# Optimization experiments

Hardware: AMD Instinct MI355X
Metric: run time of the kernel (lower is better)

The kernel has to match this reference:

```python
import jax, jax.numpy as jnp
import numpy as np

N_NODES = 100000
N_EDGES = 1600000
IN_FEATS = 128
N_HIDDEN = 128
N_CLASSES = 47


def setup_inputs() -> dict:
    key = jax.random.key(0)
    ks = jax.random.split(key, 9)
    x = jax.random.normal(ks[0], (N_NODES, IN_FEATS), dtype=jnp.float32)
    src = jax.random.randint(ks[1], (N_EDGES,), 0, N_NODES, dtype=jnp.int32)
    dst = jax.random.randint(ks[2], (N_EDGES,), 0, N_NODES, dtype=jnp.int32)
    s = 0.05
    return {
        "x": x, "src": src, "dst": dst,
        "Ws0": jax.random.normal(ks[3], (IN_FEATS, N_HIDDEN), jnp.float32) * s,
        "Wn0": jax.random.normal(ks[4], (IN_FEATS, N_HIDDEN), jnp.float32) * s,
        "b0": jnp.zeros((N_HIDDEN,), jnp.float32),
        "Ws1": jax.random.normal(ks[5], (N_HIDDEN, N_HIDDEN), jnp.float32) * s,
        "Wn1": jax.random.normal(ks[6], (N_HIDDEN, N_HIDDEN), jnp.float32) * s,
        "b1": jnp.zeros((N_HIDDEN,), jnp.float32),
        "Ws2": jax.random.normal(ks[7], (N_HIDDEN, N_CLASSES), jnp.float32) * s,
        "Wn2": jax.random.normal(ks[8], (N_HIDDEN, N_CLASSES), jnp.float32) * s,
        "b2": jnp.zeros((N_CLASSES,), jnp.float32),
    }


def _sage_layer(h, src, dst, inv_deg, Ws, Wn, b):
    # weighted (w=1) mean aggregation over in-neighbors: sum(h[src]) / in_degree
    msg = h[src]  # [E, d] irregular gather
    neigh = jax.ops.segment_sum(msg, dst, num_segments=N_NODES) * inv_deg[:, None]
    # DGL SAGEConv 'mean': fc_self(h_self) + fc_neigh(h_neigh), bias on self branch
    return h @ Ws + neigh @ Wn + b


def reference(x, src, dst, Ws0, Wn0, b0, Ws1, Wn1, b1, Ws2, Wn2, b2):
    deg = jax.ops.segment_sum(jnp.ones_like(dst, dtype=x.dtype), dst, num_segments=N_NODES)
    inv_deg = 1.0 / jnp.maximum(deg, 1.0)
    h = _sage_layer(x, src, dst, inv_deg, Ws0, Wn0, b0)
    h = jax.nn.relu(h)  # dropout is identity (eval / p=0)
    h = _sage_layer(h, src, dst, inv_deg, Ws1, Wn1, b1)
    h = jax.nn.relu(h)
    h = _sage_layer(h, src, dst, inv_deg, Ws2, Wn2, b2)
    return jax.nn.log_softmax(h, axis=-1)
```

## Files before the change

kernel.cpp:

```cpp
#include <hip/hip_runtime.h>
#include <hip/hip_bf16.h>

#define NN 100000
#define NE 1600000
#define F 128
#define NCLS 47

#define SCAN_B 98
#define NPB 256
#define BUCKETS 391
#define ABLK 512
#define ACHUNK (NE / ABLK)

typedef __attribute__((ext_vector_type(8))) short short8;
typedef __attribute__((ext_vector_type(8))) unsigned short u16x8;
typedef __attribute__((ext_vector_type(4))) float f32x4;

#define MFMA16(A, B, C) __builtin_amdgcn_mfma_f32_16x16x32_bf16(A, B, C, 0, 0, 0)

__device__ __forceinline__ unsigned short b16(float f) {
    unsigned int u = __builtin_bit_cast(unsigned int, f);
    unsigned int r = u + 0x7FFFu + ((u >> 16) & 1u);
    return (unsigned short)(r >> 16);
}
__device__ __forceinline__ float bflo(unsigned int u) { return __builtin_bit_cast(float, u << 16); }
__device__ __forceinline__ float bfhi(unsigned int u) { return __builtin_bit_cast(float, u & 0xFFFF0000u); }

__global__ void __launch_bounds__(256) k_bhist(const int* __restrict__ dst,
                                               int* __restrict__ bucket_cnt) {
    __shared__ int hist[BUCKETS];
    const int t = threadIdx.x;
    for (int i = t; i < BUCKETS; i += 256) hist[i] = 0;
    __syncthreads();
    const int e0 = blockIdx.x * ACHUNK;
    for (int i = t; i < ACHUNK; i += 256) atomicAdd(&hist[dst[e0 + i] >> 8], 1);
    __syncthreads();
    for (int i = t; i < BUCKETS; i += 256)
        if (hist[i]) atomicAdd(&bucket_cnt[i], hist[i]);
}

__global__ void k_bscan(const int* __restrict__ bucket_cnt, int* __restrict__ bucket_off,
                        int* __restrict__ cursor) {
    const int lane = threadIdx.x & 63;
    int run = 0;
#pragma unroll
    for (int c = 0; c < 7; c++) {
        int idx = c * 64 + lane;
        int v = (idx < BUCKETS) ? bucket_cnt[idx] : 0;
        int s = v;
#pragma unroll
        for (int off = 1; off < 64; off <<= 1) {
            int n = __shfl_up(s, off);
            if (lane >= off) s += n;
        }
        int excl = run + s - v;
        if (idx <= BUCKETS) {
            bucket_off[idx] = excl;
            cursor[idx] = excl;
        }
        run += __shfl(s, 63);
    }
}

__global__ void __launch_bounds__(256) k_bscatter(const int* __restrict__ src,
                                                  const int* __restrict__ dst,
                                                  int* __restrict__ cursor,
                                                  int2* __restrict__ ebuf) {
    __shared__ int hist[BUCKETS];
    __shared__ int base[BUCKETS];
    __shared__ int rank[BUCKETS];
    const int t = threadIdx.x;
    for (int i = t; i < BUCKETS; i += 256) {
        hist[i] = 0;
        rank[i] = 0;
    }
    __syncthreads();
    const int e0 = blockIdx.x * ACHUNK;
    for (int i = t; i < ACHUNK; i += 256) atomicAdd(&hist[dst[e0 + i] >> 8], 1);
    __syncthreads();
    for (int i = t; i < BUCKETS; i += 256) {
        int h = hist[i];
        base[i] = h ? atomicAdd(&cursor[i], h) : 0;
    }
    __syncthreads();
    for (int i = t; i < ACHUNK; i += 256) {
        int s = src[e0 + i];
        int d = dst[e0 + i];
        int b = d >> 8;
        int r = atomicAdd(&rank[b], 1);
        ebuf[base[b] + r] = make_int2(s, d);
    }
}

__global__ void __launch_bounds__(256) k_bdeg(const int2* __restrict__ ebuf,
                                              const int* __restrict__ bucket_off,
                                              int* __restrict__ deg) {
    __shared__ int cnt[NPB];
    const int t = threadIdx.x;
    cnt[t] = 0;
    __syncthreads();
    const int e0 = bucket_off[blockIdx.x], e1 = bucket_off[blockIdx.x + 1];
    for (int i = e0 + t; i < e1; i += 256) atomicAdd(&cnt[ebuf[i].y & 255], 1);
    __syncthreads();
    int node = (blockIdx.x << 8) + t;
    if (node < NN) deg[node] = cnt[t];
}

__global__ void __launch_bounds__(256) k_bfill(const int2* __restrict__ ebuf,
                                               const int* __restrict__ bucket_off,
                                               const int* __restrict__ row_off,
                                               int* __restrict__ col) {
    __shared__ int ro[NPB];
    __shared__ int cur[NPB];
    const int t = threadIdx.x;
    int node = (blockIdx.x << 8) + t;
    ro[t] = (node < NN) ? row_off[node] : 0;
    cur[t] = 0;
    __syncthreads();
    const int e0 = bucket_off[blockIdx.x], e1 = bucket_off[blockIdx.x + 1];
    for (int i = e0 + t; i < e1; i += 256) {
        int2 e = ebuf[i];
        int d = e.y & 255;
        int p = atomicAdd(&cur[d], 1);
        col[ro[d] + p] = e.x;
    }
}

__global__ void __launch_bounds__(256) k_part(const int* __restrict__ deg,
                                              int* __restrict__ partials) {
    __shared__ int ws[4];
    const int t = threadIdx.x, lane = t & 63, wid = t >> 6;
    int i0 = blockIdx.x * 1024 + t * 4;
    int s = 0;
    if (i0 + 3 < NN) {
        int4 v = *(const int4*)&deg[i0];
        s = v.x + v.y + v.z + v.w;
    } else {
#pragma unroll
        for (int j = 0; j < 4; j++) {
            int idx = i0 + j;
            if (idx < NN) s += deg[idx];
        }
    }
#pragma unroll
    for (int off = 1; off < 64; off <<= 1) s += __shfl_xor(s, off);
    if (lane == 0) ws[wid] = s;
    __syncthreads();
    if (t == 0) partials[blockIdx.x] = ws[0] + ws[1] + ws[2] + ws[3];
}

__global__ void k_scanpart(int* __restrict__ partials, int* __restrict__ row_off) {
    const int lane = threadIdx.x & 63;
    int v0 = (lane < SCAN_B) ? partials[lane] : 0;
    int i1 = lane + 64;
    int v1 = (i1 < SCAN_B) ? partials[i1] : 0;
    int s0 = v0;
#pragma unroll
    for (int off = 1; off < 64; off <<= 1) {
        int n = __shfl_up(s0, off);
        if (lane >= off) s0 += n;
    }
    int tot0 = __shfl(s0, 63);
    int s1 = v1;
#pragma unroll
    for (int off = 1; off < 64; off <<= 1) {
        int n = __shfl_up(s1, off);
        if (lane >= off) s1 += n;
    }
    if (lane < SCAN_B) partials[lane] = s0 - v0;
    if (i1 < SCAN_B) partials[i1] = tot0 + s1 - v1;
    if (lane == 0) row_off[NN] = NE;
}

__global__ void __launch_bounds__(256) k_offsets(const int* __restrict__ deg,
                                                 const int* __restrict__ partials,
                                                 int* __restrict__ row_off,
                                                 float* __restrict__ inv_deg) {
    __shared__ int wsum[4];
    const int t = threadIdx.x, lane = t & 63, wid = t >> 6;
    int i0 = blockIdx.x * 1024 + t * 4;
    int v[4];
    int loc = 0;
#pragma unroll
    for (int j = 0; j < 4; j++) {
        int idx = i0 + j;
        v[j] = (idx < NN) ? deg[idx] : 0;
        loc += v[j];
    }
    int run = loc;
#pragma unroll
    for (int off = 1; off < 64; off <<= 1) {
        int n = __shfl_up(run, off);
        if (lane >= off) run += n;
    }
    if (lane == 63) wsum[wid] = run;
    __syncthreads();
    int woff = partials[blockIdx.x];
#pragma unroll
    for (int wv = 0; wv < 4; wv++)
        if (wv < wid) woff += wsum[wv];
    int excl = woff + run - loc;
#pragma unroll
    for (int j = 0; j < 4; j++) {
        int idx = i0 + j;
        if (idx < NN) {
            row_off[idx] = excl;
            inv_deg[idx] = 1.0f / fmaxf((float)v[j], 1.0f);
            excl += v[j];
        }
    }
}

__global__ void k_cvt(const float* __restrict__ x, unsigned short* __restrict__ xb) {
    int t = blockIdx.x * blockDim.x + threadIdx.x;
    if (t >= NN * F / 8) return;
    const float4* x4 = (const float4*)x;
    float4 a = x4[t * 2], b = x4[t * 2 + 1];
    u16x8 o;
    o[0] = b16(a.x); o[1] = b16(a.y); o[2] = b16(a.z); o[3] = b16(a.w);
    o[4] = b16(b.x); o[5] = b16(b.y); o[6] = b16(b.z); o[7] = b16(b.w);
    ((u16x8*)xb)[t] = o;
}

__global__ void k_pack_all(const float* __restrict__ Ws0, const float* __restrict__ Wn0,
                           const float* __restrict__ Ws1, const float* __restrict__ Wn1,
                           const float* __restrict__ Ws2, const float* __restrict__ Wn2,
                           unsigned short* __restrict__ wp) {
    int idx = blockIdx.x * blockDim.x + threadIdx.x;
    if (idx >= 77824) return;
    const float* W;
    int base, ncols;
    if (idx < 65536) {
        int m = idx >> 14;
        W = (m == 0) ? Ws0 : (m == 1) ? Wn0 : (m == 2) ? Ws1 : Wn1;
        base = m << 14;
        ncols = 128;
    } else {
        int m = (idx - 65536) / 6144;
        W = m ? Wn2 : Ws2;
        base = 65536 + m * 6144;
        ncols = NCLS;
    }
    int li = idx - base;
    int nt = li >> 11;
    int r = li & 2047;
    int kk = r >> 9;
    int r2 = r & 511;
    int lane = r2 >> 3;
    int j = r2 & 7;
    int k = kk * 32 + ((lane >> 4) << 3) + j;
    int n = nt * 16 + (lane & 15);
    float v = (n < ncols) ? W[k * ncols + n] : 0.f;
    wp[idx] = b16(v);
}

__global__ void __launch_bounds__(256) k_aggb(const uint4* __restrict__ h4,
                                              const int* __restrict__ row_off,
                                              const int* __restrict__ col,
                                              const float* __restrict__ inv_deg,
                                              uint4* __restrict__ a4) {
    int node = (blockIdx.x * blockDim.x + threadIdx.x) >> 6;
    int lane = threadIdx.x & 63;
    if (node >= NN) return;
    int b = row_off[node], e = row_off[node + 1];
    int deg = e - b;
    const int g = lane >> 4, fl = lane & 15;
    float acc[8];
#pragma unroll
    for (int i = 0; i < 8; i++) acc[i] = 0.f;
    for (int base = 0; base < deg; base += 64) {
        int cnt = deg - base;
        if (cnt > 64) cnt = 64;
        int myc = col[b + base + (lane < cnt ? lane : 0)];
        for (int jj = 0; jj < cnt; jj += 16) {
            uint4 u[4];
#pragma unroll
            for (int k2 = 0; k2 < 4; k2++) {
                int r = jj + k2 * 4 + g;
                int c = __shfl(myc, r < cnt ? r : 0);
                u[k2] = h4[(size_t)(unsigned)c * 16u + fl];
            }
#pragma unroll
            for (int k2 = 0; k2 < 4; k2++) {
                int r = jj + k2 * 4 + g;
                unsigned m = (r < cnt) ? 0xFFFFFFFFu : 0u;
                uint4 v = u[k2];
                v.x &= m; v.y &= m; v.z &= m; v.w &= m;
                acc[0] += bflo(v.x); acc[1] += bfhi(v.x);
                acc[2] += bflo(v.y); acc[3] += bfhi(v.y);
                acc[4] += bflo(v.z); acc[5] += bfhi(v.z);
                acc[6] += bflo(v.w); acc[7] += bfhi(v.w);
            }
        }
    }
#pragma unroll
    for (int i = 0; i < 8; i++) {
        acc[i] += __shfl_xor(acc[i], 16);
        acc[i] += __shfl_xor(acc[i], 32);
    }
    if (g == 0) {
        float s = inv_deg[node];
        uint4 o;
        o.x = (unsigned)b16(acc[0] * s) | ((unsigned)b16(acc[1] * s) << 16);
        o.y = (unsigned)b16(acc[2] * s) | ((unsigned)b16(acc[3] * s) << 16);
        o.z = (unsigned)b16(acc[4] * s) | ((unsigned)b16(acc[5] * s) << 16);
        o.w = (unsigned)b16(acc[6] * s) | ((unsigned)b16(acc[7] * s) << 16);
        a4[(size_t)node * 16 + fl] = o;
    }
}

__global__ void __launch_bounds__(256) k_agg48(const uint4* __restrict__ hw4,
                                               const int* __restrict__ row_off,
                                               const int* __restrict__ col,
                                               const float* __restrict__ inv_deg,
                                               float4* __restrict__ aggf4) {
    int node = (blockIdx.x * blockDim.x + threadIdx.x) >> 6;
    int lane = threadIdx.x & 63;
    if (node >= NN) return;
    int b = row_off[node], e = row_off[node + 1];
    int deg = e - b;
    const int g = lane >> 3, fl = lane & 7;
    float acc[8];
#pragma unroll
    for (int i = 0; i < 8; i++) acc[i] = 0.f;
    for (int base = 0; base < deg; base += 64) {
        int cnt = deg - base;
        if (cnt > 64) cnt = 64;
        int myc = col[b + base + (lane < cnt ? lane : 0)];
        for (int jj = 0; jj < cnt; jj += 16) {
            uint4 u[2];
#pragma unroll
            for (int k2 = 0; k2 < 2; k2++) {
                int r = jj + k2 * 8 + g;
                int c = __shfl(myc, r < cnt ? r : 0);
                u[k2] = hw4[(size_t)(unsigned)c * 8u + fl];
            }
#pragma unroll
            for (int k2 = 0; k2 < 2; k2++) {
                int r = jj + k2 * 8 + g;
                unsigned m = (r < cnt) ? 0xFFFFFFFFu : 0u;
                uint4 v = u[k2];
                v.x &= m; v.y &= m; v.z &= m; v.w &= m;
                acc[0] += bflo(v.x); acc[1] += bfhi(v.x);
                acc[2] += bflo(v.y); acc[3] += bfhi(v.y);
                acc[4] += bflo(v.z); acc[5] += bfhi(v.z);
                acc[6] += bflo(v.w); acc[7] += bfhi(v.w);
            }
        }
    }
#pragma unroll
    for (int i = 0; i < 8; i++) {
        acc[i] += __shfl_xor(acc[i], 8);
        acc[i] += __shfl_xor(acc[i], 16);
        acc[i] += __shfl_xor(acc[i], 32);
    }
    if (lane < 8) {
        float s = inv_deg[node];
        float4 o0 = make_float4(acc[0] * s, acc[1] * s, acc[2] * s, acc[3] * s);
        float4 o1 = make_float4(acc[4] * s, acc[5] * s, acc[6] * s, acc[7] * s);
        aggf4[(size_t)node * 16 + fl * 2] = o0;
        aggf4[(size_t)node * 16 + fl * 2 + 1] = o1;
    }
}

template <bool RELU>
__global__ void __launch_bounds__(256) k_layer(const unsigned short* __restrict__ hb,
                                               const unsigned short* __restrict__ ab,
                                               const unsigned short* __restrict__ wps,
                                               const unsigned short* __restrict__ wpn,
                                               const float* __restrict__ bias,
                                               unsigned short* __restrict__ outb) {
    const int wid = threadIdx.x >> 6, lane = threadIdx.x & 63;
    const int tile0 = blockIdx.x * 64;
    const short8* ws8 = (const short8*)wps;
    const short8* wn8 = (const short8*)wpn;
    short8 wf[2][2][4];
#pragma unroll
    for (int t = 0; t < 2; t++) {
        int nt = 2 * wid + t;
#pragma unroll
        for (int kk = 0; kk < 4; kk++) {
            wf[0][t][kk] = ws8[(nt * 4 + kk) * 64 + lane];
            wf[1][t][kk] = wn8[(nt * 4 + kk) * 64 + lane];
        }
    }
    const int rb = lane & 15, kq = lane >> 4;
    float bv[2];
#pragma unroll
    for (int t = 0; t < 2; t++) bv[t] = bias[(2 * wid + t) * 16 + rb];
    const short8* h8 = (const short8*)hb;
    const short8* a8 = (const short8*)ab;
    f32x4 zero = {0.f, 0.f, 0.f, 0.f};
    f32x4 acc[4][2];
#pragma unroll
    for (int m = 0; m < 4; m++)
#pragma unroll
        for (int t = 0; t < 2; t++) acc[m][t] = zero;
#pragma unroll
    for (int kk = 0; kk < 4; kk++) {
#pragma unroll
        for (int m = 0; m < 4; m++) {
            int row = tile0 + m * 16 + rb;
            int rc = row < NN ? row : NN - 1;
            int idx = rc * 16 + kk * 4 + kq;
            short8 af = h8[idx];
            short8 gf = a8[idx];
            acc[m][0] = MFMA16(af, wf[0][0][kk], acc[m][0]);
            acc[m][1] = MFMA16(af, wf[0][1][kk], acc[m][1]);
            acc[m][0] = MFMA16(gf, wf[1][0][kk], acc[m][0]);
            acc[m][1] = MFMA16(gf, wf[1][1][kk], acc[m][1]);
        }
    }
#pragma unroll
    for (int m = 0; m < 4; m++) {
#pragma unroll
        for (int reg = 0; reg < 4; reg++) {
            int row = tile0 + m * 16 + kq * 4 + reg;
            if (row < NN) {
#pragma unroll
                for (int t = 0; t < 2; t++) {
                    float v = acc[m][t][reg] + bv[t];
                    if (RELU) v = fmaxf(v, 0.f);
                    outb[(size_t)row * F + (2 * wid + t) * 16 + rb] = b16(v);
                }
            }
        }
    }
}

__global__ void __launch_bounds__(512) k_nmul(const unsigned short* __restrict__ hb,
                                              const unsigned short* __restrict__ wpn,
                                              unsigned short* __restrict__ hw) {
    const int wid = threadIdx.x >> 6, lane = threadIdx.x & 63;
    const int R0 = blockIdx.x * 128 + wid * 16;
    const short8* wn8 = (const short8*)wpn;
    short8 wf[3][4];
#pragma unroll
    for (int nt = 0; nt < 3; nt++)
#pragma unroll
        for (int kk = 0; kk < 4; kk++) wf[nt][kk] = wn8[(nt * 4 + kk) * 64 + lane];
    const int rb = lane & 15, kq = lane >> 4;
    const short8* h8 = (const short8*)hb;
    f32x4 zero = {0.f, 0.f, 0.f, 0.f};
    f32x4 acc[3] = {zero, zero, zero};
    int rowr = R0 + rb;
    int rc = rowr < NN ? rowr : NN - 1;
#pragma unroll
    for (int kk = 0; kk < 4; kk++) {
        short8 af = h8[rc * 16 + kk * 4 + kq];
#pragma unroll
        for (int nt = 0; nt < 3; nt++) acc[nt] = MFMA16(af, wf[nt][kk], acc[nt]);
    }
#pragma unroll
    for (int reg = 0; reg < 4; reg++) {
        int row = R0 + kq * 4 + reg;
        if (row < NN) {
#pragma unroll
            for (int nt = 0; nt < 3; nt++)
                hw[(size_t)row * 64 + nt * 16 + rb] = b16(acc[nt][reg]);
        }
    }
}

__global__ void __launch_bounds__(512) k_out2(const unsigned short* __restrict__ hb,
                                              const float* __restrict__ aggf,
                                              const unsigned short* __restrict__ wps,
                                              const float* __restrict__ bias,
                                              float* __restrict__ out) {
    const int wid = threadIdx.x >> 6, lane = threadIdx.x & 63;
    const int R0 = blockIdx.x * 128 + wid * 16;
    const short8* ws8 = (const short8*)wps;
    short8 wf[3][4];
#pragma unroll
    for (int nt = 0; nt < 3; nt++)
#pragma unroll
        for (int kk = 0; kk < 4; kk++) wf[nt][kk] = ws8[(nt * 4 + kk) * 64 + lane];
    const int rb = lane & 15, kq = lane >> 4;
    float bv[3];
    bool valid[3];
#pragma unroll
    for (int nt = 0; nt < 3; nt++) {
        int c = nt * 16 + rb;
        valid[nt] = c < NCLS;
        bv[nt] = valid[nt] ? bias[c] : 0.f;
    }
    const short8* h8 = (const short8*)hb;
    f32x4 zero = {0.f, 0.f, 0.f, 0.f};
    f32x4 acc[3] = {zero, zero, zero};
    int rowr = R0 + rb;
    int rc = rowr < NN ? rowr : NN - 1;
#pragma unroll
    for (int kk = 0; kk < 4; kk++) {
        short8 af = h8[rc * 16 + kk * 4 + kq];
#pragma unroll
        for (int nt = 0; nt < 3; nt++) acc[nt] = MFMA16(af, wf[nt][kk], acc[nt]);
    }
#pragma unroll
    for (int reg = 0; reg < 4; reg++) {
        int row = R0 + kq * 4 + reg;
        int rc2 = row < NN ? row : NN - 1;
        float v[3];
        float mx = -1e30f;
#pragma unroll
        for (int nt = 0; nt < 3; nt++) {
            float av = aggf[(size_t)rc2 * 64 + nt * 16 + rb];
            v[nt] = acc[nt][reg] + av + bv[nt];
            if (valid[nt]) mx = fmaxf(mx, v[nt]);
        }
        for (int off = 1; off < 16; off <<= 1) mx = fmaxf(mx, __shfl_xor(mx, off));
        float s = 0.f;
#pragma unroll
        for (int nt = 0; nt < 3; nt++)
            if (valid[nt]) s += expf(v[nt] - mx);
        for (int off = 1; off < 16; off <<= 1) s += __shfl_xor(s, off);
        float L = mx + logf(s);
        if (row < NN) {
#pragma unroll
            for (int nt = 0; nt < 3; nt++)
                if (valid[nt]) out[(size_t)row * NCLS + nt * 16 + rb] = v[nt] - L;
        }
    }
}

extern "C" void kernel_launch(void* const* d_in, const int* in_sizes, int n_in,
                              void* d_out, int out_size, void* d_ws, size_t ws_size,
                              hipStream_t stream) {
    (void)in_sizes; (void)n_in; (void)out_size; (void)ws_size;
    const float* x = (const float*)d_in[0];
    const int* src = (const int*)d_in[1];
    const int* dst = (const int*)d_in[2];
    const float* Ws0 = (const float*)d_in[3];
    const float* Wn0 = (const float*)d_in[4];
    const float* b0 = (const float*)d_in[5];
    const float* Ws1 = (const float*)d_in[6];
    const float* Wn1 = (const float*)d_in[7];
    const float* b1 = (const float*)d_in[8];
    const float* Ws2 = (const float*)d_in[9];
    const float* Wn2 = (const float*)d_in[10];
    const float* b2 = (const float*)d_in[11];
    float* out = (float*)d_out;

    char* w = (char*)d_ws;
    size_t off = 0;
    auto alloc = [&](size_t bytes) -> char* {
        char* p = w + off;
        off = (off + bytes + 255) & ~(size_t)255;
        return p;
    };
    int* deg = (int*)alloc((size_t)NN * 4);
    int* row_off = (int*)alloc((size_t)(NN + 1) * 4);
    int* col = (int*)alloc((size_t)NE * 4);
    float* inv_deg = (float*)alloc((size_t)NN * 4);
    int* partials = (int*)alloc((size_t)SCAN_B * 4);
    int* bucket_cnt = (int*)alloc((size_t)(BUCKETS + 1) * 4);
    int* bucket_off = (int*)alloc((size_t)(BUCKETS + 1) * 4);
    int* bcursor = (int*)alloc((size_t)(BUCKETS + 1) * 4);
    int2* ebuf = (int2*)alloc((size_t)NE * 8);
    unsigned short* xb = (unsigned short*)alloc((size_t)NN * F * 2);
    unsigned short* aggb = (unsigned short*)alloc((size_t)NN * F * 2);
    unsigned short* h1b = (unsigned short*)alloc((size_t)NN * F * 2);
    unsigned short* h2b = (unsigned short*)alloc((size_t)NN * F * 2);
    unsigned short* wp = (unsigned short*)alloc((size_t)77824 * 2);

    unsigned short* hw2b = (unsigned short*)ebuf;
    float* agg2f = (float*)aggb;

    hipMemsetAsync(bucket_cnt, 0, (size_t)(BUCKETS + 1) * 4, stream);

    k_bhist<<<ABLK, 256, 0, stream>>>(dst, bucket_cnt);
    k_bscan<<<1, 64, 0, stream>>>(bucket_cnt, bucket_off, bcursor);
    k_bscatter<<<ABLK, 256, 0, stream>>>(src, dst, bcursor, ebuf);
    k_bdeg<<<BUCKETS, 256, 0, stream>>>(ebuf, bucket_off, deg);
    k_part<<<SCAN_B, 256, 0, stream>>>(deg, partials);
    k_scanpart<<<1, 64, 0, stream>>>(partials, row_off);
    k_offsets<<<SCAN_B, 256, 0, stream>>>(deg, partials, row_off, inv_deg);
    k_bfill<<<BUCKETS, 256, 0, stream>>>(ebuf, bucket_off, row_off, col);

    k_cvt<<<(NN * F / 8 + 255) / 256, 256, 0, stream>>>(x, xb);
    k_pack_all<<<(77824 + 255) / 256, 256, 0, stream>>>(Ws0, Wn0, Ws1, Wn1, Ws2, Wn2, wp);

    unsigned short* wS0 = wp;
    unsigned short* wN0 = wp + 16384;
    unsigned short* wS1 = wp + 32768;
    unsigned short* wN1 = wp + 49152;
    unsigned short* wS2 = wp + 65536;
    unsigned short* wN2 = wp + 71680;

    const int AGG_B = NN * 64 / 256;
    const int LYR_B = (NN + 63) / 64;
    const int OUT_B = (NN + 127) / 128;

    k_aggb<<<AGG_B, 256, 0, stream>>>((const uint4*)xb, row_off, col, inv_deg, (uint4*)aggb);
    k_layer<true><<<LYR_B, 256, 0, stream>>>(xb, aggb, wS0, wN0, b0, h1b);
    k_aggb<<<AGG_B, 256, 0, stream>>>((const uint4*)h1b, row_off, col, inv_deg, (uint4*)aggb);
    k_layer<true><<<LYR_B, 256, 0, stream>>>(h1b, aggb, wS1, wN1, b1, h2b);
    k_nmul<<<OUT_B, 512, 0, stream>>>(h2b, wN2, hw2b);
    k_agg48<<<AGG_B, 256, 0, stream>>>((const uint4*)hw2b, row_off, col, inv_deg,
                                       (float4*)agg2f);
    k_out2<<<OUT_B, 512, 0, stream>>>(h2b, agg2f, wS2, b2, out);
}
```

Baseline: 334.0 us.

## Fuse CSR build kernels per bucket and use zero-pad row for masked gathers

Merges the degree count, global prefix scan, offset/inv_deg computation and column fill into a single per-bucket kernel. The global scan becomes unnecessary because bucket_off already gives each bucket's edge base, so each block only scans its own 256 nodes. This removes four kernel launches and the deg/partials round trips. Separately, the aggregation kernels now redirect out-of-range lanes to a zeroed padding row at index NN instead of masking the loaded values. That saves the AND instructions at the cost of a small zero-fill kernel and extra padded allocations.

```diff
diff --git a/kernel.cpp b/kernel.cpp
--- a/kernel.cpp
+++ b/kernel.cpp
@@ -6,7 +6,6 @@
 #define F 128
 #define NCLS 47
 
-#define SCAN_B 98
 #define NPB 256
 #define BUCKETS 391
 #define ABLK 512
@@ -92,122 +91,48 @@
     }
 }
 
-__global__ void __launch_bounds__(256) k_bdeg(const int2* __restrict__ ebuf,
+__global__ void __launch_bounds__(256) k_bcsr(const int2* __restrict__ ebuf,
                                               const int* __restrict__ bucket_off,
-                                              int* __restrict__ deg) {
+                                              int* __restrict__ row_off,
+                                              float* __restrict__ inv_deg,
+                                              int* __restrict__ col) {
     __shared__ int cnt[NPB];
-    const int t = threadIdx.x;
+    __shared__ int ro[NPB];
+    __shared__ int wsum[4];
+    const int t = threadIdx.x, lane = t & 63, wid = t >> 6;
     cnt[t] = 0;
     __syncthreads();
     const int e0 = bucket_off[blockIdx.x], e1 = bucket_off[blockIdx.x + 1];
     for (int i = e0 + t; i < e1; i += 256) atomicAdd(&cnt[ebuf[i].y & 255], 1);
     __syncthreads();
+    int v = cnt[t];
+    int run = v;
+#pragma unroll
+    for (int off = 1; off < 64; off <<= 1) {
+        int n = __shfl_up(run, off);
+        if (lane >= off) run += n;
+    }
+    if (lane == 63) wsum[wid] = run;
+    __syncthreads();
+    int woff = e0;
+#pragma unroll
+    for (int wv = 0; wv < 4; wv++)
+        if (wv < wid) woff += wsum[wv];
+    int excl = woff + run - v;
     int node = (blockIdx.x << 8) + t;
-    if (node < NN) deg[node] = cnt[t];
-}
-
-__global__ void __launch_bounds__(256) k_bfill(const int2* __restrict__ ebuf,
-                                               const int* __restrict__ bucket_off,
-                                               const int* __restrict__ row_off,
-                                               int* __restrict__ col) {
-    __shared__ int ro[NPB];
-    __shared__ int cur[NPB];
-    const int t = threadIdx.x;
-    int node = (blockIdx.x << 8) + t;
-    ro[t] = (node < NN) ? row_off[node] : 0;
-    cur[t] = 0;
-    __syncthreads();
-    const int e0 = bucket_off[blockIdx.x], e1 = bucket_off[blockIdx.x + 1];
+    if (node < NN) {
+        row_off[node] = excl;
+        inv_deg[node] = 1.0f / fmaxf((float)v, 1.0f);
+    }
+    if (blockIdx.x == BUCKETS - 1 && t == 0) row_off[NN] = NE;
+    ro[t] = excl;
+    cnt[t] = 0;
+    __syncthreads();
     for (int i = e0 + t; i < e1; i += 256) {
         int2 e = ebuf[i];
         int d = e.y & 255;
-        int p = atomicAdd(&cur[d], 1);
+        int p = atomicAdd(&cnt[d], 1);
         col[ro[d] + p] = e.x;
-    }
-}
-
-__global__ void __launch_bounds__(256) k_part(const int* __restrict__ deg,
-                                              int* __restrict__ partials) {
-    __shared__ int ws[4];
-    const int t = threadIdx.x, lane = t & 63, wid = t >> 6;
-    int i0 = blockIdx.x * 1024 + t * 4;
-    int s = 0;
-    if (i0 + 3 < NN) {
-        int4 v = *(const int4*)&deg[i0];
-        s = v.x + v.y + v.z + v.w;
-    } else {
-#pragma unroll
-        for (int j = 0; j < 4; j++) {
-            int idx = i0 + j;
-            if (idx < NN) s += deg[idx];
-        }
-    }
-#pragma unroll
-    for (int off = 1; off < 64; off <<= 1) s += __shfl_xor(s, off);
-    if (lane == 0) ws[wid] = s;
-    __syncthreads();
-    if (t == 0) partials[blockIdx.x] = ws[0] + ws[1] + ws[2] + ws[3];
-}
-
-__global__ void k_scanpart(int* __restrict__ partials, int* __restrict__ row_off) {
-    const int lane = threadIdx.x & 63;
-    int v0 = (lane < SCAN_B) ? partials[lane] : 0;
-    int i1 = lane + 64;
-    int v1 = (i1 < SCAN_B) ? partials[i1] : 0;
-    int s0 = v0;
-#pragma unroll
-    for (int off = 1; off < 64; off <<= 1) {
-        int n = __shfl_up(s0, off);
-        if (lane >= off) s0 += n;
-    }
-    int tot0 = __shfl(s0, 63);
-    int s1 = v1;
-#pragma unroll
-    for (int off = 1; off < 64; off <<= 1) {
-        int n = __shfl_up(s1, off);
-        if (lane >= off) s1 += n;
-    }
-    if (lane < SCAN_B) partials[lane] = s0 - v0;
-    if (i1 < SCAN_B) partials[i1] = tot0 + s1 - v1;
-    if (lane == 0) row_off[NN] = NE;
-}
-
-__global__ void __launch_bounds__(256) k_offsets(const int* __restrict__ deg,
-                                                 const int* __restrict__ partials,
-                                                 int* __restrict__ row_off,
-                                                 float* __restrict__ inv_deg) {
-    __shared__ int wsum[4];
-    const int t = threadIdx.x, lane = t & 63, wid = t >> 6;
-    int i0 = blockIdx.x * 1024 + t * 4;
-    int v[4];
-    int loc = 0;
-#pragma unroll
-    for (int j = 0; j < 4; j++) {
-        int idx = i0 + j;
-        v[j] = (idx < NN) ? deg[idx] : 0;
-        loc += v[j];
-    }
-    int run = loc;
-#pragma unroll
-    for (int off = 1; off < 64; off <<= 1) {
-        int n = __shfl_up(run, off);
-        if (lane >= off) run += n;
-    }
-    if (lane == 63) wsum[wid] = run;
-    __syncthreads();
-    int woff = partials[blockIdx.x];
-#pragma unroll
-    for (int wv = 0; wv < 4; wv++)
-        if (wv < wid) woff += wsum[wv];
-    int excl = woff + run - loc;
-#pragma unroll
-    for (int j = 0; j < 4; j++) {
-        int idx = i0 + j;
-        if (idx < NN) {
-            row_off[idx] = excl;
-            inv_deg[idx] = 1.0f / fmaxf((float)v[j], 1.0f);
-            excl += v[j];
-        }
     }
 }
 
@@ -220,6 +145,14 @@
     o[0] = b16(a.x); o[1] = b16(a.y); o[2] = b16(a.z); o[3] = b16(a.w);
     o[4] = b16(b.x); o[5] = b16(b.y); o[6] = b16(b.z); o[7] = b16(b.w);
     ((u16x8*)xb)[t] = o;
+}
+
+__global__ void k_zpad(unsigned short* __restrict__ xb, unsigned short* __restrict__ h1b,
+                       unsigned short* __restrict__ hw2b) {
+    int t = threadIdx.x;
+    xb[(size_t)NN * F + t] = 0;
+    h1b[(size_t)NN * F + t] = 0;
+    if (t < 64) hw2b[(size_t)NN * 64 + t] = 0;
 }
 
 __global__ void k_pack_all(const float* __restrict__ Ws0, const float* __restrict__ Wn0,
@@ -277,15 +210,13 @@
 #pragma unroll
             for (int k2 = 0; k2 < 4; k2++) {
                 int r = jj + k2 * 4 + g;
-                int c = __shfl(myc, r < cnt ? r : 0);
+                int c = __shfl(myc, r);
+                c = (r < cnt) ? c : NN;
                 u[k2] = h4[(size_t)(unsigned)c * 16u + fl];
             }
 #pragma unroll
             for (int k2 = 0; k2 < 4; k2++) {
-                int r = jj + k2 * 4 + g;
-                unsigned m = (r < cnt) ? 0xFFFFFFFFu : 0u;
                 uint4 v = u[k2];
-                v.x &= m; v.y &= m; v.z &= m; v.w &= m;
                 acc[0] += bflo(v.x); acc[1] += bfhi(v.x);
                 acc[2] += bflo(v.y); acc[3] += bfhi(v.y);
                 acc[4] += bflo(v.z); acc[5] += bfhi(v.z);
@@ -332,15 +263,13 @@
 #pragma unroll
             for (int k2 = 0; k2 < 2; k2++) {
                 int r = jj + k2 * 8 + g;
-                int c = __shfl(myc, r < cnt ? r : 0);
+                int c = __shfl(myc, r);
+                c = (r < cnt) ? c : NN;
                 u[k2] = hw4[(size_t)(unsigned)c * 8u + fl];
             }
 #pragma unroll
             for (int k2 = 0; k2 < 2; k2++) {
-                int r = jj + k2 * 8 + g;
-                unsigned m = (r < cnt) ? 0xFFFFFFFFu : 0u;
                 uint4 v = u[k2];
-                v.x &= m; v.y &= m; v.z &= m; v.w &= m;
                 acc[0] += bflo(v.x); acc[1] += bfhi(v.x);
                 acc[2] += bflo(v.y); acc[3] += bfhi(v.y);
                 acc[4] += bflo(v.z); acc[5] += bfhi(v.z);
@@ -547,18 +476,16 @@
         off = (off + bytes + 255) & ~(size_t)255;
         return p;
     };
-    int* deg = (int*)alloc((size_t)NN * 4);
     int* row_off = (int*)alloc((size_t)(NN + 1) * 4);
     int* col = (int*)alloc((size_t)NE * 4);
     float* inv_deg = (float*)alloc((size_t)NN * 4);
-    int* partials = (int*)alloc((size_t)SCAN_B * 4);
     int* bucket_cnt = (int*)alloc((size_t)(BUCKETS + 1) * 4);
     int* bucket_off = (int*)alloc((size_t)(BUCKETS + 1) * 4);
     int* bcursor = (int*)alloc((size_t)(BUCKETS + 1) * 4);
-    int2* ebuf = (int2*)alloc((size_t)NE * 8);
-    unsigned short* xb = (unsigned short*)alloc((size_t)NN * F * 2);
+    int2* ebuf = (int2*)alloc((size_t)NE * 8 + 256);
+    unsigned short* xb = (unsigned short*)alloc((size_t)(NN + 1) * F * 2);
     unsigned short* aggb = (unsigned short*)alloc((size_t)NN * F * 2);
-    unsigned short* h1b = (unsigned short*)alloc((size_t)NN * F * 2);
+    unsigned short* h1b = (unsigned short*)alloc((size_t)(NN + 1) * F * 2);
     unsigned short* h2b = (unsigned short*)alloc((size_t)NN * F * 2);
     unsigned short* wp = (unsigned short*)alloc((size_t)77824 * 2);
 
@@ -570,11 +497,7 @@
     k_bhist<<<ABLK, 256, 0, stream>>>(dst, bucket_cnt);
     k_bscan<<<1, 64, 0, stream>>>(bucket_cnt, bucket_off, bcursor);
     k_bscatter<<<ABLK, 256, 0, stream>>>(src, dst, bcursor, ebuf);
-    k_bdeg<<<BUCKETS, 256, 0, stream>>>(ebuf, bucket_off, deg);
-    k_part<<<SCAN_B, 256, 0, stream>>>(deg, partials);
-    k_scanpart<<<1, 64, 0, stream>>>(partials, row_off);
-    k_offsets<<<SCAN_B, 256, 0, stream>>>(deg, partials, row_off, inv_deg);
-    k_bfill<<<BUCKETS, 256, 0, stream>>>(ebuf, bucket_off, row_off, col);
+    k_bcsr<<<BUCKETS, 256, 0, stream>>>(ebuf, bucket_off, row_off, inv_deg, col);
 
     k_cvt<<<(NN * F / 8 + 255) / 256, 256, 0, stream>>>(x, xb);
     k_pack_all<<<(77824 + 255) / 256, 256, 0, stream>>>(Ws0, Wn0, Ws1, Wn1, Ws2, Wn2, wp);
@@ -589,6 +512,8 @@
     const int AGG_B = NN * 64 / 256;
     const int LYR_B = (NN + 63) / 64;
     const int OUT_B = (NN + 127) / 128;
+
+    k_zpad<<<1, 128, 0, stream>>>(xb, h1b, hw2b);
 
     k_aggb<<<AGG_B, 256, 0, stream>>>((const uint4*)xb, row_off, col, inv_deg, (uint4*)aggb);
     k_layer<true><<<LYR_B, 256, 0, stream>>>(xb, aggb, wS0, wN0, b0, h1b);
```

Result: faster. 325.7 us (-2.5%).
